# Optimization experiments

Hardware: AMD Instinct MI355X
Metric: run time of the kernel (lower is better)

## Reference

```python
import jax, jax.numpy as jnp
import numpy as np


def setup_inputs() -> dict:
    key = jax.random.key(0)
    k1, k2 = jax.random.split(key)
    B, N, M = 8, 8192, 8192
    points1 = jax.random.normal(k1, (B, N, 2), dtype=jnp.float32)
    points2 = jax.random.normal(k2, (B, M, 2), dtype=jnp.float32)
    return {"points1": points1, "points2": points2}


def reference(points1, points2):
    # points1: [B, N, 2], points2: [B, M, 2]
    # Squared pairwise distances via |a|^2 + |b|^2 - 2 a.b  -> [B, N, M]
    p1_sq = jnp.sum(points1 * points1, axis=-1)  # [B, N]
    p2_sq = jnp.sum(points2 * points2, axis=-1)  # [B, M]
    cross = jnp.einsum("bnd,bmd->bnm", points1, points2)  # [B, N, M]
    sqdist = p1_sq[:, :, None] + p2_sq[:, None, :] - 2.0 * cross
    dist1 = jnp.min(sqdist, axis=2)  # [B, N]: NN of each p1 point in p2
    dist2 = jnp.min(sqdist, axis=1)  # [B, M]: NN of each p2 point in p1
    cost = jnp.mean(dist1, axis=-1) + jnp.mean(dist2, axis=-1)  # [B]
    return jnp.sum(cost)
```

## Files before the change

### kernel.cpp

```cpp
#include <hip/hip_runtime.h>


#define BATCH 8
#define NPTS  8192
#define TPB   256
#define IPT   16
#define PPB   (TPB * IPT)
#define TILES (NPTS / PPB)
#define S     16
#define JCH   (NPTS / S)

__global__ __launch_bounds__(TPB, 2)
void chamfer_partial(const float* __restrict__ p1, const float* __restrict__ p2,
                     float* __restrict__ partial ) {
    __shared__ float4 q[JCH];

    int blk = blockIdx.x;
    int split = blk & (S - 1);      blk >>= 4;
    int tile  = blk & (TILES - 1);  blk >>= 1;
    int b     = blk & (BATCH - 1);  blk >>= 3;
    int dir   = blk;

    const float2* a  = (const float2*)(dir ? p2 : p1) + (size_t)b * NPTS;
    const float2* bp = (const float2*)(dir ? p1 : p2) + (size_t)b * NPTS + split * JCH;

    int t = threadIdx.x;

    for (int j = t; j < JCH; j += TPB) {
        float2 v = bp[j];
        q[j] = make_float4(v.x, v.y, fmaf(v.x, v.x, v.y * v.y), 0.0f);
    }

    int pt_base = tile * PPB;
    float xp[IPT], yp[IPT], m[IPT];
#pragma unroll
    for (int k = 0; k < IPT; ++k) {
        float2 v = a[pt_base + k * TPB + t];
        xp[k] = -2.0f * v.x;
        yp[k] = -2.0f * v.y;
        m[k]  = 3.0e38f;
    }

    __syncthreads();

    for (int j = 0; j < JCH; j += 2) {
        float4 q0 = q[j];
        float4 q1 = q[j + 1];
#pragma unroll
        for (int k = 0; k < IPT; ++k) {
            float t0 = fmaf(yp[k], q0.y, fmaf(xp[k], q0.x, q0.z));
            float t1 = fmaf(yp[k], q1.y, fmaf(xp[k], q1.x, q1.z));
            m[k] = fminf(m[k], fminf(t0, t1));
        }
    }

    float* out = partial + ((size_t)(dir * BATCH + b) * S + split) * NPTS + pt_base;
#pragma unroll
    for (int k = 0; k < IPT; ++k)
        out[k * TPB + t] = m[k];
}

__global__ __launch_bounds__(TPB)
void chamfer_reduce(const float* __restrict__ p1, const float* __restrict__ p2,
                    const float* __restrict__ partial, float* __restrict__ out) {
    int gid   = blockIdx.x * TPB + threadIdx.x;
    int point = gid & (NPTS - 1);
    int rest  = gid >> 13;
    int b     = rest & (BATCH - 1);
    int dir   = rest >> 3;

    const float* base = partial + ((size_t)(dir * BATCH + b) * S) * NPTS + point;
    float m = base[0];
#pragma unroll
    for (int s = 1; s < S; ++s)
        m = fminf(m, base[(size_t)s * NPTS]);

    float2 v = ((const float2*)(dir ? p2 : p1))[(size_t)b * NPTS + point];
    float d = m + fmaf(v.x, v.x, v.y * v.y);

#pragma unroll
    for (int off = 32; off > 0; off >>= 1)
        d += __shfl_down(d, off, 64);

    __shared__ float wsum[TPB / 64];
    int lane = threadIdx.x & 63;
    int w    = threadIdx.x >> 6;
    if (lane == 0) wsum[w] = d;
    __syncthreads();
    if (threadIdx.x == 0) {
        float ssum = wsum[0] + wsum[1] + wsum[2] + wsum[3];
        atomicAdd(out, ssum * (1.0f / NPTS));
    }
}

extern "C" void kernel_launch(void* const* d_in, const int* in_sizes, int n_in,
                              void* d_out, int out_size, void* d_ws, size_t ws_size,
                              hipStream_t stream) {
    const float* p1 = (const float*)d_in[0];
    const float* p2 = (const float*)d_in[1];
    float* out      = (float*)d_out;
    float* partial  = (float*)d_ws;

    hipMemsetAsync(d_out, 0, sizeof(float), stream);

    chamfer_partial<<<2 * BATCH * TILES * S, TPB, 0, stream>>>(p1, p2, partial);
    chamfer_reduce<<<2 * BATCH * NPTS / TPB, TPB, 0, stream>>>(p1, p2, partial, out);
}
```

Baseline: 138.4 us.

## Use v_min3 inline asm, double split count, raise occupancy, drop memset

Replaces the pairwise fminf chain with the v_min3_f32 instruction so that each two candidate distances cost one min op, and unrolls the inner loop over 8 shared-memory points. Doubles the split factor to 32, which halves the LDS chunk per block, and raises launch bounds to 4 blocks per SM for more parallelism and occupancy. Zeroes the output inside the first kernel instead of with a separate memset launch. The costs are a larger partial buffer and more reduce work, and the occupancy hint may create register pressure with 16 accumulators plus 8 float4 values.

```diff
diff --git a/kernel.cpp b/kernel.cpp
--- a/kernel.cpp
+++ b/kernel.cpp
@@ -7,16 +7,25 @@
 #define IPT   16
 #define PPB   (TPB * IPT)
 #define TILES (NPTS / PPB)
-#define S     16
+#define S     32
 #define JCH   (NPTS / S)
 
-__global__ __launch_bounds__(TPB, 2)
+__device__ inline float min3f(float a, float b, float c) {
+    float d;
+    asm("v_min3_f32 %0, %1, %2, %3" : "=v"(d) : "v"(a), "v"(b), "v"(c));
+    return d;
+}
+
+__global__ __launch_bounds__(TPB, 4)
 void chamfer_partial(const float* __restrict__ p1, const float* __restrict__ p2,
-                     float* __restrict__ partial ) {
+                     float* __restrict__ partial ,
+                     float* __restrict__ out_to_zero) {
     __shared__ float4 q[JCH];
 
-    int blk = blockIdx.x;
-    int split = blk & (S - 1);      blk >>= 4;
+    if (blockIdx.x == 0 && threadIdx.x == 0) *out_to_zero = 0.0f;
+
+    int blk   = blockIdx.x;
+    int split = blk & (S - 1);      blk >>= 5;
     int tile  = blk & (TILES - 1);  blk >>= 1;
     int b     = blk & (BATCH - 1);  blk >>= 3;
     int dir   = blk;
@@ -43,21 +52,30 @@
 
     __syncthreads();
 
-    for (int j = 0; j < JCH; j += 2) {
-        float4 q0 = q[j];
-        float4 q1 = q[j + 1];
+    for (int j = 0; j < JCH; j += 8) {
+        float4 q0 = q[j + 0], q1 = q[j + 1], q2 = q[j + 2], q3 = q[j + 3];
+        float4 q4 = q[j + 4], q5 = q[j + 5], q6 = q[j + 6], q7 = q[j + 7];
 #pragma unroll
         for (int k = 0; k < IPT; ++k) {
             float t0 = fmaf(yp[k], q0.y, fmaf(xp[k], q0.x, q0.z));
             float t1 = fmaf(yp[k], q1.y, fmaf(xp[k], q1.x, q1.z));
-            m[k] = fminf(m[k], fminf(t0, t1));
+            float t2 = fmaf(yp[k], q2.y, fmaf(xp[k], q2.x, q2.z));
+            float t3 = fmaf(yp[k], q3.y, fmaf(xp[k], q3.x, q3.z));
+            float t4 = fmaf(yp[k], q4.y, fmaf(xp[k], q4.x, q4.z));
+            float t5 = fmaf(yp[k], q5.y, fmaf(xp[k], q5.x, q5.z));
+            float t6 = fmaf(yp[k], q6.y, fmaf(xp[k], q6.x, q6.z));
+            float t7 = fmaf(yp[k], q7.y, fmaf(xp[k], q7.x, q7.z));
+            m[k] = min3f(m[k], t0, t1);
+            m[k] = min3f(m[k], t2, t3);
+            m[k] = min3f(m[k], t4, t5);
+            m[k] = min3f(m[k], t6, t7);
         }
     }
 
-    float* out = partial + ((size_t)(dir * BATCH + b) * S + split) * NPTS + pt_base;
+    float* outp = partial + ((size_t)((dir * BATCH + b) * S + split)) * NPTS + pt_base;
 #pragma unroll
     for (int k = 0; k < IPT; ++k)
-        out[k * TPB + t] = m[k];
+        outp[k * TPB + t] = m[k];
 }
 
 __global__ __launch_bounds__(TPB)
@@ -101,8 +119,6 @@
     float* out      = (float*)d_out;
     float* partial  = (float*)d_ws;
 
-    hipMemsetAsync(d_out, 0, sizeof(float), stream);
-
-    chamfer_partial<<<2 * BATCH * TILES * S, TPB, 0, stream>>>(p1, p2, partial);
+    chamfer_partial<<<2 * BATCH * TILES * S, TPB, 0, stream>>>(p1, p2, partial, out);
     chamfer_reduce<<<2 * BATCH * NPTS / TPB, TPB, 0, stream>>>(p1, p2, partial, out);
 }
```

Result: faster. 124.6 us (-9.9%).
